# Performance work log

Hardware: AMD Instinct MI355X
Metric: run time of the kernel (lower is better)

The kernel has to match this reference:

```python
import jax, jax.numpy as jnp
import numpy as np

N, C_A, C_S, C_Z, H = 1024, 768, 384, 128, 16
D = C_A // H  # 48


def _ln(x, gamma=None, beta=None, eps=1e-5):
    m = jnp.mean(x, axis=-1, keepdims=True)
    v = jnp.var(x, axis=-1, keepdims=True)
    y = (x - m) * jax.lax.rsqrt(v + eps)
    if gamma is not None:
        y = y * gamma
    if beta is not None:
        y = y + beta
    return y


def _adaln(a, s, gamma_s, Wg, bg, Wadd):
    # AF3 Algorithm 26: LN(a) w/o affine, LN(s) w/ scale only; gate + additive shift from s
    a_ln = _ln(a)
    s_ln = _ln(s, gamma_s)
    return jax.nn.sigmoid(s_ln @ Wg + bg) * a_ln + s_ln @ Wadd


def setup_inputs() -> dict:
    key = jax.random.key(0)
    ks = iter(jax.random.split(key, 40))
    def nrm(shape, scale=0.02):
        return jax.random.normal(next(ks), shape, dtype=jnp.float32) * scale
    f32 = jnp.float32
    return dict(
        a=jax.random.normal(next(ks), (1, N, C_A), dtype=f32),
        s=jax.random.normal(next(ks), (1, N, C_S), dtype=f32),
        z=jax.random.normal(next(ks), (1, N, N, C_Z), dtype=f32),
        # AdaptiveLayerNorm (attention branch)
        gamma_s1=jnp.ones((C_S,), f32), Wg1=nrm((C_S, C_A)), bg1=jnp.zeros((C_A,), f32), Wadd1=nrm((C_S, C_A)),
        # pair-bias: LN(z) scale-only + LinearNoBias(c_z -> n_heads)
        gamma_z=jnp.ones((C_Z,), f32), Wz=nrm((C_Z, H)),
        # Attention: q has bias, k/v no bias, sigmoid gating, output proj
        Wq=nrm((C_A, C_A)), bq=jnp.zeros((C_A,), f32),
        Wk=nrm((C_A, C_A)), Wv=nrm((C_A, C_A)),
        Wgate=nrm((C_A, C_A)), bgate=jnp.ones((C_A,), f32),
        Wo=nrm((C_A, C_A)), bo=jnp.zeros((C_A,), f32),
        # BiasInitLinear output gate (biasinit=-2)
        Ws_last=nrm((C_S, C_A)), bs_last=jnp.full((C_A,), -2.0, f32),
        # ConditionedTransitionBlock (n=2)
        gamma_s2=jnp.ones((C_S,), f32), Wg2=nrm((C_S, C_A)), bg2=jnp.zeros((C_A,), f32), Wadd2=nrm((C_S, C_A)),
        W1=nrm((C_A, 2 * C_A)), W2=nrm((C_A, 2 * C_A)), Wb=nrm((2 * C_A, C_A)),
        Ws_t=nrm((C_S, C_A)), b_t=jnp.full((C_A,), -2.0, f32),
    )


def reference(a, s, z, gamma_s1, Wg1, bg1, Wadd1, gamma_z, Wz,
              Wq, bq, Wk, Wv, Wgate, bgate, Wo, bo, Ws_last, bs_last,
              gamma_s2, Wg2, bg2, Wadd2, W1, W2, Wb, Ws_t, b_t):
    B = a.shape[0]
    # ---- AttentionPairBias (standard / global path) ----
    a_ln = _adaln(a, s, gamma_s1, Wg1, bg1, Wadd1)
    bias = _ln(z, gamma_z) @ Wz                     # [B, N, N, H]
    bias = jnp.moveaxis(bias, -1, -3)               # [B, H, N, N]
    q = (a_ln @ Wq + bq).reshape(B, N, H, D)
    k = (a_ln @ Wk).reshape(B, N, H, D)
    v = (a_ln @ Wv).reshape(B, N, H, D)
    scale = 1.0 / float(np.sqrt(D))
    scores = jnp.einsum('bqhd,bkhd->bhqk', q, k) * scale + bias
    attn = jax.nn.softmax(scores, axis=-1)
    o = jnp.einsum('bhqk,bkhd->bqhd', attn, v)      # [B, N, H, D]
    g = jax.nn.sigmoid(a_ln @ Wgate + bgate).reshape(B, N, H, D)
    o = (g * o).reshape(B, N, C_A) @ Wo + bo
    attn_out = jax.nn.sigmoid(s @ Ws_last + bs_last) * o
    # ---- ConditionedTransitionBlock (Algorithm 25, n=2) ----
    a2 = _adaln(a, s, gamma_s2, Wg2, bg2, Wadd2)
    bmid = jax.nn.silu(a2 @ W1) * (a2 @ W2)
    t_out = jax.nn.sigmoid(s @ Ws_t + b_t) * (bmid @ Wb)
    # Algorithm 23 line 2-3: a = b + ConditionedTransitionBlock(a, s)
    return attn_out + t_out
```

## Files before the change

### kernel.cpp

```cpp
#include <hip/hip_runtime.h>

typedef __bf16 bf16;
typedef __bf16 v8bf __attribute__((ext_vector_type(8)));
typedef float  v4f  __attribute__((ext_vector_type(4)));
typedef short  short4v __attribute__((ext_vector_type(4)));

__device__ __forceinline__ float sigf(float x){ return 1.0f/(1.0f + __expf(-x)); }

typedef __attribute__((address_space(3))) unsigned int lds_u32;
typedef __attribute__((address_space(1))) const unsigned int gbl_u32;
__device__ __forceinline__ void gl16(const void* g, void* l) {
  __builtin_amdgcn_global_load_lds((gbl_u32*)g, (lds_u32*)l, 16, 0, 0);
}

struct WTab {
  const float* src[14];
  bf16* dst[14];
  int K[14], N[14], boff[14];
};

__global__ __launch_bounds__(256) void k_prepw(WTab tab) {
  __shared__ float lds[32][33];
  int bid = blockIdx.x;
  int e = 0;
  #pragma unroll
  for (int i = 1; i < 14; i++) if (tab.boff[i] <= bid) e = i;
  int local = bid - tab.boff[e];
  int K = tab.K[e], N = tab.N[e];
  int nKT = K >> 5;
  int kt = local % nKT, nt = local / nKT;
  int k0 = kt * 32, n0 = nt * 32;
  const float* src = tab.src[e];
  bf16* dst = tab.dst[e];
  int tx = threadIdx.x & 31, ty = threadIdx.x >> 5;
  #pragma unroll
  for (int i = 0; i < 4; i++)
    lds[ty + i*8][tx] = src[(long)(k0 + ty + i*8) * N + n0 + tx];
  __syncthreads();
  #pragma unroll
  for (int i = 0; i < 4; i++)
    dst[(long)(n0 + ty + i*8) * K + k0 + tx] = (bf16)lds[tx][ty + i*8];
}

__global__ void k_prepz(const float* __restrict__ Wz, const float* __restrict__ gz,
                        bf16* __restrict__ wzT) {
  int t = blockIdx.x * 256 + threadIdx.x;
  int k = t >> 4, h = t & 15;
  wzT[h * 128 + k] = (bf16)(Wz[t] * gz[k]);
}

__global__ __launch_bounds__(256) void k_ln_a(const float* __restrict__ a,
                                              float* __restrict__ out) {
  int row = blockIdx.x;
  const float* x = a + (long)row * 768;
  int t = threadIdx.x;
  float lv[3], s = 0.f, q = 0.f;
  #pragma unroll
  for (int i = 0; i < 3; i++){ lv[i] = x[t + i*256]; s += lv[i]; q += lv[i]*lv[i]; }
  #pragma unroll
  for (int m = 1; m < 64; m <<= 1){ s += __shfl_xor(s, m); q += __shfl_xor(q, m); }
  __shared__ float ls[4], lq[4];
  int w = t >> 6, lane = t & 63;
  if (!lane){ ls[w] = s; lq[w] = q; }
  __syncthreads();
  s = ls[0]+ls[1]+ls[2]+ls[3]; q = lq[0]+lq[1]+lq[2]+lq[3];
  float mean = s * (1.f/768.f);
  float var  = q * (1.f/768.f) - mean*mean;
  float inv  = rsqrtf(var + 1e-5f);
  float* o = out + (long)row * 768;
  #pragma unroll
  for (int i = 0; i < 3; i++) o[t + i*256] = (lv[i] - mean) * inv;
}

__global__ __launch_bounds__(128) void k_ln_s(const float* __restrict__ sIn,
    const float* __restrict__ g1, const float* __restrict__ g2,
    bf16* __restrict__ s1, bf16* __restrict__ s2, bf16* __restrict__ sb) {
  int row = blockIdx.x;
  const float* x = sIn + (long)row * 384;
  int t = threadIdx.x;
  float lv[3], s = 0.f, q = 0.f;
  #pragma unroll
  for (int i = 0; i < 3; i++){ lv[i] = x[t + i*128]; s += lv[i]; q += lv[i]*lv[i]; }
  #pragma unroll
  for (int m = 1; m < 64; m <<= 1){ s += __shfl_xor(s, m); q += __shfl_xor(q, m); }
  __shared__ float ls[2], lq[2];
  int w = t >> 6, lane = t & 63;
  if (!lane){ ls[w] = s; lq[w] = q; }
  __syncthreads();
  s = ls[0] + ls[1]; q = lq[0] + lq[1];
  float mean = s * (1.f/384.f);
  float var  = q * (1.f/384.f) - mean*mean;
  float inv  = rsqrtf(var + 1e-5f);
  long base = (long)row * 384;
  #pragma unroll
  for (int i = 0; i < 3; i++){
    int c = t + i*128;
    float y = (lv[i] - mean) * inv;
    s1[base + c] = (bf16)(y * g1[c]);
    s2[base + c] = (bf16)(y * g2[c]);
    sb[base + c] = (bf16)lv[i];
  }
}

__global__ __launch_bounds__(256) void k_zbias(const float* __restrict__ z,
    const bf16* __restrict__ wzT, bf16* __restrict__ biasb) {
  __shared__ float pb[64][17];
  int t = threadIdx.x, lane = t & 63, w = t >> 6;
  int r16 = lane & 15, g4 = lane >> 4;
  long base = (long)blockIdx.x * 64;
  long pos = base + w*16 + r16;
  const float* zr = z + pos * 128;
  float4 xv[8];
  #pragma unroll
  for (int s = 0; s < 4; s++) {
    xv[2*s]   = *reinterpret_cast<const float4*>(&zr[s*32 + g4*8]);
    xv[2*s+1] = *reinterpret_cast<const float4*>(&zr[s*32 + g4*8 + 4]);
  }
  const float* x = reinterpret_cast<const float*>(xv);
  float sm = 0.f, q = 0.f;
  #pragma unroll
  for (int i = 0; i < 32; i++){ sm += x[i]; q += x[i]*x[i]; }
  sm += __shfl_xor(sm, 16); q += __shfl_xor(q, 16);
  sm += __shfl_xor(sm, 32); q += __shfl_xor(q, 32);
  float mean = sm * (1.f/128.f), var = q * (1.f/128.f) - mean*mean;
  float inv = rsqrtf(var + 1e-5f);
  v4f acc = (v4f){0.f, 0.f, 0.f, 0.f};
  #pragma unroll
  for (int s = 0; s < 4; s++) {
    union { bf16 b[8]; v8bf v; } ua;
    #pragma unroll
    for (int j = 0; j < 8; j++) ua.b[j] = (bf16)((x[s*8 + j] - mean) * inv);
    v8bf bw = *reinterpret_cast<const v8bf*>(&wzT[r16*128 + s*32 + g4*8]);
    acc = __builtin_amdgcn_mfma_f32_16x16x32_bf16(ua.v, bw, acc, 0, 0, 0);
  }
  #pragma unroll
  for (int r = 0; r < 4; r++) pb[w*16 + g4*4 + r][r16] = acc[r];
  __syncthreads();
  int p = t & 63, hb = t >> 6;
  #pragma unroll
  for (int j = 0; j < 4; j++) {
    int h = hb*4 + j;
    biasb[((long)h << 20) + base + p] = (bf16)pb[p][h];
  }
}

#define EPI_ADASG  0
#define EPI_SWIGLU 1
#define EPI_QKVG   2
#define EPI_WO     6
#define EPI_WB     7

template<int TM, int TN, bool DUAL, int EPI>
__global__ __launch_bounds__(256) void gemm_k(
    const bf16* __restrict__ A, const bf16* __restrict__ B,
    long sAz, long sBz, long sBpair, int K,
    const float* __restrict__ f0, const float* __restrict__ f1,
    const float* __restrict__ f2, const float* __restrict__ f3,
    const float* __restrict__ f4, const bf16* __restrict__ bb0,
    void* __restrict__ outp, long sOutz)
{
  constexpr int WM = TM/2, WN = TN/2;
  constexpr int MI = WM/16, NI = WN/16;
  __shared__ __align__(16) bf16 As[TM*64];
  __shared__ __align__(16) bf16 Bs[(DUAL?2:1)*TN*64];
  int z = blockIdx.z;
  const bf16* Ap = A + (long)z * sAz;
  const bf16* B1 = B + (long)z * sBz;
  const bf16* B2 = B1 + sBpair;
  int m0 = blockIdx.y * TM, n0 = blockIdx.x * TN;
  int t = threadIdx.x, lane = t & 63, w = t >> 6;
  int wr = w >> 1, wc = w & 1;
  int r16 = lane & 15, g4 = lane >> 4;
  constexpr int NACC = DUAL ? 2 : 1;
  v4f acc[NACC][MI][NI];
  #pragma unroll
  for (int d = 0; d < NACC; d++)
    #pragma unroll
    for (int mi = 0; mi < MI; mi++)
      #pragma unroll
      for (int ni = 0; ni < NI; ni++)
        acc[d][mi][ni] = (v4f){0.f, 0.f, 0.f, 0.f};

  for (int k0 = 0; k0 < K; k0 += 64) {
    #pragma unroll
    for (int cb = 0; cb < TM/32; cb++) {
      int cc = cb*4 + w;
      int c16 = cc*64 + lane;
      int row = c16 >> 3, col = c16 & 7;
      int scol = col ^ (row & 7);
      gl16(&Ap[(long)(m0 + row)*K + k0 + scol*8], (char*)As + cc*1024);
    }
    #pragma unroll
    for (int cb = 0; cb < TN/32; cb++) {
      int cc = cb*4 + w;
      int c16 = cc*64 + lane;
      int row = c16 >> 3, col = c16 & 7;
      int scol = col ^ (row & 7);
      gl16(&B1[(long)(n0 + row)*K + k0 + scol*8], (char*)Bs + cc*1024);
      if constexpr (DUAL)
        gl16(&B2[(long)(n0 + row)*K + k0 + scol*8], (char*)Bs + TN*128 + cc*1024);
    }
    __syncthreads();
    #pragma unroll
    for (int s = 0; s < 2; s++) {
      int ch = s*4 + g4;
      v8bf af[MI];
      #pragma unroll
      for (int mi = 0; mi < MI; mi++) {
        int ra = wr*WM + mi*16 + r16;
        af[mi] = *reinterpret_cast<const v8bf*>(
            (const char*)As + ra*128 + ((ch ^ (ra & 7)) << 4));
      }
      #pragma unroll
      for (int d = 0; d < NACC; d++)
        #pragma unroll
        for (int ni = 0; ni < NI; ni++) {
          int rb = wc*WN + ni*16 + r16;
          v8bf bfv = *reinterpret_cast<const v8bf*>(
              (const char*)Bs + d*(TN*128) + rb*128 + ((ch ^ (rb & 7)) << 4));
          #pragma unroll
          for (int mi = 0; mi < MI; mi++)
            acc[d][mi][ni] = __builtin_amdgcn_mfma_f32_16x16x32_bf16(af[mi], bfv, acc[d][mi][ni], 0, 0, 0);
        }
    }
    __syncthreads();
  }

  int colb = n0 + wc*WN + r16;
  int rowb = m0 + wr*WM + (g4 << 2);
  #pragma unroll
  for (int mi = 0; mi < MI; mi++)
    #pragma unroll
    for (int ni = 0; ni < NI; ni++) {
      int col = colb + ni*16;
      if constexpr (EPI == EPI_ADASG) {
        if (z < 2) {
          float bg = (z == 0 ? f1 : f2)[col];
          bf16* o = (bf16*)outp + (long)z * sOutz;
          #pragma unroll
          for (int r = 0; r < 4; r++) {
            long idx = (long)(rowb + mi*16 + r)*768 + col;
            float gl = acc[0][mi][ni][r] + bg;
            o[idx] = (bf16)(sigf(gl) * f0[idx] + acc[1][mi][ni][r]);
          }
        } else {
          bf16* o0 = (bf16*)outp + 2*sOutz;
          bf16* o1 = (bf16*)outp + 3*sOutz;
          #pragma unroll
          for (int r = 0; r < 4; r++) {
            long idx = (long)(rowb + mi*16 + r)*768 + col;
            o0[idx] = (bf16)sigf(acc[0][mi][ni][r] + f3[col]);
            o1[idx] = (bf16)sigf(acc[1][mi][ni][r] + f4[col]);
          }
        }
      } else if constexpr (EPI == EPI_SWIGLU) {
        bf16* o = (bf16*)outp;
        #pragma unroll
        for (int r = 0; r < 4; r++) {
          long idx = (long)(rowb + mi*16 + r)*1536 + col;
          float x1 = acc[0][mi][ni][r], x2 = acc[1][mi][ni][r];
          o[idx] = (bf16)(x1 * sigf(x1) * x2);
        }
      } else if constexpr (EPI == EPI_QKVG) {
        int h = col / 48, d = col - h*48;
        if (z == 0) {
          const float qs = 0.14433756729740643f;
          bf16* qp = (bf16*)outp;
          #pragma unroll
          for (int r = 0; r < 4; r++)
            qp[(long)h*65536 + (long)(rowb + mi*16 + r)*64 + d] =
              (bf16)((acc[0][mi][ni][r] + f0[col]) * qs);
        } else if (z == 1) {
          bf16* kp = (bf16*)outp + sOutz;
          #pragma unroll
          for (int r = 0; r < 4; r++)
            kp[(long)h*65536 + (long)(rowb + mi*16 + r)*64 + d] = (bf16)acc[0][mi][ni][r];
        } else if (z == 2) {
          bf16* vT = (bf16*)outp + 2*sOutz;
          union { bf16 h4[4]; short4v s4; } u;
          #pragma unroll
          for (int r = 0; r < 4; r++) u.h4[r] = (bf16)acc[0][mi][ni][r];
          *reinterpret_cast<short4v*>(&vT[(long)h*65536 + (long)d*1024 + rowb + mi*16]) = u.s4;
        } else {
          bf16* gp = (bf16*)outp + 3*sOutz;
          #pragma unroll
          for (int r = 0; r < 4; r++)
            gp[(long)(rowb + mi*16 + r)*768 + col] = (bf16)sigf(acc[0][mi][ni][r] + f1[col]);
        }
      } else if constexpr (EPI == EPI_WO) {
        float* o = (float*)outp;
        #pragma unroll
        for (int r = 0; r < 4; r++) {
          long idx = (long)(rowb + mi*16 + r)*768 + col;
          o[idx] = (float)bb0[idx] * (acc[0][mi][ni][r] + f0[col]);
        }
      } else {
        float* o = (float*)outp;
        #pragma unroll
        for (int r = 0; r < 4; r++) {
          long idx = (long)(rowb + mi*16 + r)*768 + col;
          o[idx] = f0[idx] + (float)bb0[idx] * acc[0][mi][ni][r];
        }
      }
    }
}

__global__ __launch_bounds__(256) void k_flash(
    const bf16* __restrict__ qp, const bf16* __restrict__ kp,
    const bf16* __restrict__ vT, const bf16* __restrict__ biasb,
    const bf16* __restrict__ gp, bf16* __restrict__ gob)
{
  __shared__ bf16 pl[4][16*72];
  int t = threadIdx.x, lane = t & 63, w = t >> 6;
  int h = blockIdx.y;
  int q0 = blockIdx.x * 64 + w * 16;
  int r16 = lane & 15, g4 = lane >> 4;
  const bf16* qb = qp + ((long)h << 16);
  const bf16* kb = kp + ((long)h << 16);
  const bf16* vb = vT + ((long)h << 16);
  const bf16* bb = biasb + ((long)h << 20) + (long)q0 * 1024;

  v8bf qa[2];
  #pragma unroll
  for (int s = 0; s < 2; s++)
    qa[s] = *reinterpret_cast<const v8bf*>(&qb[(long)(q0 + r16)*64 + s*32 + g4*8]);

  v4f oacc[4];
  #pragma unroll
  for (int nd = 0; nd < 4; nd++) oacc[nd] = (v4f){0.f, 0.f, 0.f, 0.f};
  float mrun[4], lrun[4];
  #pragma unroll
  for (int r = 0; r < 4; r++){ mrun[r] = -1e30f; lrun[r] = 0.f; }

  for (int kt = 0; kt < 16; kt++) {
    int k0 = kt * 64;
    v4f sacc[4];
    #pragma unroll
    for (int nk = 0; nk < 4; nk++) sacc[nk] = (v4f){0.f, 0.f, 0.f, 0.f};
    #pragma unroll
    for (int nk = 0; nk < 4; nk++)
      #pragma unroll
      for (int s = 0; s < 2; s++) {
        v8bf kf = *reinterpret_cast<const v8bf*>(&kb[(long)(k0 + nk*16 + r16)*64 + s*32 + g4*8]);
        sacc[nk] = __builtin_amdgcn_mfma_f32_16x16x32_bf16(qa[s], kf, sacc[nk], 0, 0, 0);
      }
    float mtile[4];
    #pragma unroll
    for (int r = 0; r < 4; r++) mtile[r] = -1e30f;
    #pragma unroll
    for (int nk = 0; nk < 4; nk++)
      #pragma unroll
      for (int r = 0; r < 4; r++) {
        float bvv = (float)bb[(long)(g4*4 + r)*1024 + k0 + nk*16 + r16];
        sacc[nk][r] += bvv;
        mtile[r] = fmaxf(mtile[r], sacc[nk][r]);
      }
    #pragma unroll
    for (int r = 0; r < 4; r++) {
      #pragma unroll
      for (int m = 1; m < 16; m <<= 1) mtile[r] = fmaxf(mtile[r], __shfl_xor(mtile[r], m));
    }
    float scl[4], rsum[4];
    #pragma unroll
    for (int r = 0; r < 4; r++) {
      float mn = fmaxf(mrun[r], mtile[r]);
      scl[r] = __expf(mrun[r] - mn);
      mrun[r] = mn;
      rsum[r] = 0.f;
    }
    bf16* plw = &pl[w][0];
    #pragma unroll
    for (int nk = 0; nk < 4; nk++)
      #pragma unroll
      for (int r = 0; r < 4; r++) {
        float p = __expf(sacc[nk][r] - mrun[r]);
        rsum[r] += p;
        plw[(g4*4 + r)*72 + nk*16 + r16] = (bf16)p;
      }
    #pragma unroll
    for (int r = 0; r < 4; r++) {
      #pragma unroll
      for (int m = 1; m < 16; m <<= 1) rsum[r] += __shfl_xor(rsum[r], m);
      lrun[r] = lrun[r]*scl[r] + rsum[r];
      #pragma unroll
      for (int nd = 0; nd < 4; nd++) oacc[nd][r] *= scl[r];
    }
    v8bf pa[2];
    #pragma unroll
    for (int s = 0; s < 2; s++)
      pa[s] = *reinterpret_cast<const v8bf*>(&plw[r16*72 + s*32 + g4*8]);
    #pragma unroll
    for (int nd = 0; nd < 4; nd++)
      #pragma unroll
      for (int s = 0; s < 2; s++) {
        v8bf vf = *reinterpret_cast<const v8bf*>(&vb[(long)(nd*16 + r16)*1024 + k0 + s*32 + g4*8]);
        oacc[nd] = __builtin_amdgcn_mfma_f32_16x16x32_bf16(pa[s], vf, oacc[nd], 0, 0, 0);
      }
  }
  #pragma unroll
  for (int r = 0; r < 4; r++) {
    int qrow = q0 + g4*4 + r;
    float invl = 1.0f / lrun[r];
    #pragma unroll
    for (int nd = 0; nd < 3; nd++) {
      long idx = (long)qrow*768 + h*48 + nd*16 + r16;
      gob[idx] = (bf16)(oacc[nd][r] * invl * (float)gp[idx]);
    }
  }
}

extern "C" void kernel_launch(void* const* d_in, const int* in_sizes, int n_in,
                              void* d_out, int out_size, void* d_ws, size_t ws_size,
                              hipStream_t stream)
{
  const float* A_in  = (const float*)d_in[0];
  const float* S_in  = (const float*)d_in[1];
  const float* Z_in  = (const float*)d_in[2];
  const float* g_s1  = (const float*)d_in[3];
  const float* Wg1   = (const float*)d_in[4];
  const float* bg1   = (const float*)d_in[5];
  const float* Wadd1 = (const float*)d_in[6];
  const float* g_z   = (const float*)d_in[7];
  const float* Wz    = (const float*)d_in[8];
  const float* Wq    = (const float*)d_in[9];
  const float* bq    = (const float*)d_in[10];
  const float* Wk    = (const float*)d_in[11];
  const float* Wv    = (const float*)d_in[12];
  const float* Wgate = (const float*)d_in[13];
  const float* bgate = (const float*)d_in[14];
  const float* Wo    = (const float*)d_in[15];
  const float* bo    = (const float*)d_in[16];
  const float* WsL   = (const float*)d_in[17];
  const float* bsL   = (const float*)d_in[18];
  const float* g_s2  = (const float*)d_in[19];
  const float* Wg2   = (const float*)d_in[20];
  const float* bg2   = (const float*)d_in[21];
  const float* Wadd2 = (const float*)d_in[22];
  const float* W1    = (const float*)d_in[23];
  const float* W2    = (const float*)d_in[24];
  const float* Wb    = (const float*)d_in[25];
  const float* WsT   = (const float*)d_in[26];
  const float* b_t   = (const float*)d_in[27];
  float* OUT = (float*)d_out;

  char* ws = (char*)d_ws;
  size_t off = 0;
  auto alloc = [&](size_t bytes) -> void* {
    void* p = ws + off; off += (bytes + 255) & ~(size_t)255; return p; };

  bf16*  wGA6  = (bf16*) alloc(6ul*294912*2);
  bf16*  wQKVG = (bf16*) alloc(4ul*589824*2);
  bf16*  wWoT  = (bf16*) alloc(589824ul*2);
  bf16*  wW12  = (bf16*) alloc(2ul*1179648*2);
  bf16*  wWbT  = (bf16*) alloc(1179648ul*2);
  bf16*  wzT   = (bf16*) alloc(2048ul*2);
  bf16*  sl1   = (bf16*) alloc(393216ul*2);
  bf16*  sl2   = (bf16*) alloc(393216ul*2);
  bf16*  sbf   = (bf16*) alloc(393216ul*2);
  float* alnr  = (float*)alloc(786432ul*4);
  bf16*  aln   = (bf16*) alloc(786432ul*2);
  bf16*  a2b   = (bf16*) alloc(786432ul*2);
  bf16*  sgf   = (bf16*) alloc(2ul*786432*2);
  bf16*  qkv   = (bf16*) alloc((3ul*1048576 + 786432)*2);
  bf16*  biasb = (bf16*) alloc(16777216ul*2);
  bf16*  gob   = (bf16*) alloc(786432ul*2);
  float* opj   = (float*)alloc(786432ul*4);
  bf16*  bmid  = (bf16*) alloc(1572864ul*2);

  WTab tab;
  auto setw = [&](int i, const float* src, bf16* dst, int K, int N){
    tab.src[i] = src; tab.dst[i] = dst; tab.K[i] = K; tab.N[i] = N; };
  setw(0,  Wg1,   wGA6,             384,  768);
  setw(1,  Wadd1, wGA6 + 294912,    384,  768);
  setw(2,  Wg2,   wGA6 + 589824,    384,  768);
  setw(3,  Wadd2, wGA6 + 884736,    384,  768);
  setw(4,  WsL,   wGA6 + 1179648,   384,  768);
  setw(5,  WsT,   wGA6 + 1474560,   384,  768);
  setw(6,  Wq,    wQKVG,            768,  768);
  setw(7,  Wk,    wQKVG + 589824,   768,  768);
  setw(8,  Wv,    wQKVG + 2*589824, 768,  768);
  setw(9,  Wgate, wQKVG + 3*589824, 768,  768);
  setw(10, Wo,    wWoT,             768,  768);
  setw(11, W1,    wW12,             768, 1536);
  setw(12, W2,    wW12 + 1179648,   768, 1536);
  setw(13, Wb,    wWbT,            1536,  768);
  int boff = 0;
  for (int i = 0; i < 14; i++){ tab.boff[i] = boff; boff += (tab.K[i]/32)*(tab.N[i]/32); }

  k_prepw<<<boff, 256, 0, stream>>>(tab);
  k_prepz<<<8, 256, 0, stream>>>(Wz, g_z, wzT);
  k_ln_a<<<1024, 256, 0, stream>>>(A_in, alnr);
  k_ln_s<<<1024, 128, 0, stream>>>(S_in, g_s1, g_s2, sl1, sl2, sbf);
  (void)hipMemsetAsync(qkv, 0, 3ul*1048576*2, stream);
  k_zbias<<<16384, 256, 0, stream>>>(Z_in, wzT, biasb);

  gemm_k<64,64,true,EPI_ADASG><<<dim3(12,16,3), 256, 0, stream>>>(
      sl1, wGA6, 393216, 589824, 294912, 384,
      alnr, bg1, bg2, bsL, b_t, nullptr, aln, 786432);

  gemm_k<64,64,false,EPI_QKVG><<<dim3(12,16,4), 256, 0, stream>>>(
      aln, wQKVG, 0, 589824, 0, 768,
      bq, bgate, nullptr, nullptr, nullptr, nullptr, qkv, 1048576);

  k_flash<<<dim3(16,16), 256, 0, stream>>>(
      qkv, qkv + 1048576, qkv + 2097152, biasb, qkv + 3145728, gob);

  gemm_k<64,64,false,EPI_WO><<<dim3(12,16,1), 256, 0, stream>>>(
      gob, wWoT, 0, 0, 0, 768,
      bo, nullptr, nullptr, nullptr, nullptr, sgf, opj, 0);

  gemm_k<64,64,true,EPI_SWIGLU><<<dim3(24,16,1), 256, 0, stream>>>(
      a2b, wW12, 0, 0, 1179648, 768,
      nullptr, nullptr, nullptr, nullptr, nullptr, nullptr, bmid, 0);

  gemm_k<64,64,false,EPI_WB><<<dim3(12,16,1), 256, 0, stream>>>(
      bmid, wWbT, 0, 0, 0, 1536,
      opj, nullptr, nullptr, nullptr, nullptr, sgf + 786432, OUT, 0);
}
```

Measured before the change: 261.3 us.

## Merge QKVG GEMM, SwiGLU GEMM and z-bias into one heterogeneous launch

Refactors the GEMM and z-bias kernels into device bodies and dispatches them from a single mega-kernel by block index. The 768 QKVG GEMM tiles, the 384 SwiGLU tiles and the 16384 memory-bound z-bias blocks share one grid, so the compute-bound GEMMs can overlap with streaming z and launch gaps are removed. Shared memory is a single 24KB buffer sized for the dual GEMM, so occupancy for the z-bias blocks is limited by that footprint. The z-bias work now runs after the AdaLN GEMM instead of before it, which moves it later in the stream order.

```diff
diff --git a/kernel.cpp b/kernel.cpp
--- a/kernel.cpp
+++ b/kernel.cpp
@@ -102,12 +102,13 @@
   }
 }
 
-__global__ __launch_bounds__(256) void k_zbias(const float* __restrict__ z,
-    const bf16* __restrict__ wzT, bf16* __restrict__ biasb) {
-  __shared__ float pb[64][17];
+__device__ __forceinline__ void zbias_body(int bid, char* smem,
+    const float* __restrict__ z, const bf16* __restrict__ wzT,
+    bf16* __restrict__ biasb) {
+  float (*pb)[17] = (float(*)[17])smem;
   int t = threadIdx.x, lane = t & 63, w = t >> 6;
   int r16 = lane & 15, g4 = lane >> 4;
-  long base = (long)blockIdx.x * 64;
+  long base = (long)bid * 64;
   long pos = base + w*16 + r16;
   const float* zr = z + pos * 128;
   float4 xv[8];
@@ -151,9 +152,9 @@
 #define EPI_WB     7
 
 template<int TM, int TN, bool DUAL, int EPI>
-__global__ __launch_bounds__(256) void gemm_k(
-    const bf16* __restrict__ A, const bf16* __restrict__ B,
-    long sAz, long sBz, long sBpair, int K,
+__device__ __forceinline__ void gemm_body(
+    bf16* As, bf16* Bs, int m0, int n0, int z,
+    const bf16* __restrict__ Ap, const bf16* __restrict__ B1, long sBpair, int K,
     const float* __restrict__ f0, const float* __restrict__ f1,
     const float* __restrict__ f2, const float* __restrict__ f3,
     const float* __restrict__ f4, const bf16* __restrict__ bb0,
@@ -161,13 +162,7 @@
 {
   constexpr int WM = TM/2, WN = TN/2;
   constexpr int MI = WM/16, NI = WN/16;
-  __shared__ __align__(16) bf16 As[TM*64];
-  __shared__ __align__(16) bf16 Bs[(DUAL?2:1)*TN*64];
-  int z = blockIdx.z;
-  const bf16* Ap = A + (long)z * sAz;
-  const bf16* B1 = B + (long)z * sBz;
   const bf16* B2 = B1 + sBpair;
-  int m0 = blockIdx.y * TM, n0 = blockIdx.x * TN;
   int t = threadIdx.x, lane = t & 63, w = t >> 6;
   int wr = w >> 1, wc = w & 1;
   int r16 = lane & 15, g4 = lane >> 4;
@@ -303,6 +298,44 @@
         }
       }
     }
+}
+
+template<int TM, int TN, bool DUAL, int EPI>
+__global__ __launch_bounds__(256) void gemm_k(
+    const bf16* A, const bf16* B, long sAz, long sBz, long sBpair, int K,
+    const float* f0, const float* f1, const float* f2, const float* f3,
+    const float* f4, const bf16* bb0, void* outp, long sOutz)
+{
+  __shared__ __align__(16) bf16 As[TM*64];
+  __shared__ __align__(16) bf16 Bs[(DUAL?2:1)*TN*64];
+  int z = blockIdx.z;
+  gemm_body<TM,TN,DUAL,EPI>(As, Bs, blockIdx.y*TM, blockIdx.x*TN, z,
+      A + (long)z*sAz, B + (long)z*sBz, sBpair, K,
+      f0, f1, f2, f3, f4, bb0, outp, sOutz);
+}
+
+__global__ __launch_bounds__(256, 4) void k_mega(
+    const bf16* aln, const bf16* wQKVG, const float* bq, const float* bgate,
+    bf16* qkv, const bf16* a2b, const bf16* wW12, bf16* bmid,
+    const float* Zin, const bf16* wzT, bf16* biasb)
+{
+  __shared__ __align__(16) char smem[24576];
+  int bid = blockIdx.x;
+  if (bid < 768) {
+    int z = bid / 192, rem = bid % 192;
+    gemm_body<64,64,false,EPI_QKVG>((bf16*)smem, (bf16*)(smem + 8192),
+        (rem/12)*64, (rem%12)*64, z,
+        aln, wQKVG + (long)z*589824, 0, 768,
+        bq, bgate, nullptr, nullptr, nullptr, nullptr, qkv, 1048576);
+  } else if (bid < 1152) {
+    int rem = bid - 768;
+    gemm_body<64,64,true,EPI_SWIGLU>((bf16*)smem, (bf16*)(smem + 8192),
+        (rem/24)*64, (rem%24)*64, 0,
+        a2b, wW12, 1179648, 768,
+        nullptr, nullptr, nullptr, nullptr, nullptr, nullptr, bmid, 0);
+  } else {
+    zbias_body(bid - 1152, smem, Zin, wzT, biasb);
+  }
 }
 
 __global__ __launch_bounds__(256) void k_flash(
@@ -492,15 +525,13 @@
   k_ln_a<<<1024, 256, 0, stream>>>(A_in, alnr);
   k_ln_s<<<1024, 128, 0, stream>>>(S_in, g_s1, g_s2, sl1, sl2, sbf);
   (void)hipMemsetAsync(qkv, 0, 3ul*1048576*2, stream);
-  k_zbias<<<16384, 256, 0, stream>>>(Z_in, wzT, biasb);
 
   gemm_k<64,64,true,EPI_ADASG><<<dim3(12,16,3), 256, 0, stream>>>(
       sl1, wGA6, 393216, 589824, 294912, 384,
       alnr, bg1, bg2, bsL, b_t, nullptr, aln, 786432);
 
-  gemm_k<64,64,false,EPI_QKVG><<<dim3(12,16,4), 256, 0, stream>>>(
-      aln, wQKVG, 0, 589824, 0, 768,
-      bq, bgate, nullptr, nullptr, nullptr, nullptr, qkv, 1048576);
+  k_mega<<<17536, 256, 0, stream>>>(
+      aln, wQKVG, bq, bgate, qkv, a2b, wW12, bmid, Z_in, wzT, biasb);
 
   k_flash<<<dim3(16,16), 256, 0, stream>>>(
       qkv, qkv + 1048576, qkv + 2097152, biasb, qkv + 3145728, gob);
@@ -509,10 +540,6 @@
       gob, wWoT, 0, 0, 0, 768,
       bo, nullptr, nullptr, nullptr, nullptr, sgf, opj, 0);
 
-  gemm_k<64,64,true,EPI_SWIGLU><<<dim3(24,16,1), 256, 0, stream>>>(
-      a2b, wW12, 0, 0, 1179648, 768,
-      nullptr, nullptr, nullptr, nullptr, nullptr, nullptr, bmid, 0);
-
   gemm_k<64,64,false,EPI_WB><<<dim3(12,16,1), 256, 0, stream>>>(
       bmid, wWbT, 0, 0, 0, 1536,
       opj, nullptr, nullptr, nullptr, nullptr, sgf + 786432, OUT, 0);
```

Measured after the change: 241.9 us. 1.08x faster.
